# Performance work log

Measured on AMD Instinct MI355X. Metric: run time of the kernel, lower is better.

The kernel has to match this reference:

```python
import jax, jax.numpy as jnp
import numpy as np

B, C_IN, C_OUT, H, W = 4, 256, 256, 64, 64
KH = KW = 3
STRIDE = 1
PAD = 1
DIL = 1


def setup_inputs() -> dict:
    key = jax.random.key(0)
    k1, k2, k3, k4 = jax.random.split(key, 4)
    x = jax.random.normal(k1, (B, C_IN, H, W), dtype=jnp.float32)
    # torchvision layout: 2*dg*KH*KW channels, (y, x) pair per kernel tap
    offset = jax.random.normal(k2, (B, 2 * KH * KW, H, W), dtype=jnp.float32)
    fan_in = C_IN * KH * KW
    weight = jax.random.normal(k3, (C_OUT, C_IN, KH, KW), dtype=jnp.float32) / np.sqrt(fan_in)
    bias = jax.random.normal(k4, (C_OUT,), dtype=jnp.float32) * 0.01
    return {"x": x, "offset": offset, "weight": weight, "bias": bias}


def _gather_bilinear_corner(x_flat, yi, xi, h, w):
    # x_flat: [B, C, H*W]; yi/xi: [B, KK, Ho, Wo] int32
    valid = ((yi >= 0) & (yi < h) & (xi >= 0) & (xi < w)).astype(x_flat.dtype)
    idx = jnp.clip(yi, 0, h - 1) * w + jnp.clip(xi, 0, w - 1)
    b = idx.shape[0]
    g = jnp.take_along_axis(x_flat, idx.reshape(b, 1, -1), axis=2)
    return g.reshape(b, x_flat.shape[1], *yi.shape[1:]), valid


def deform_conv2d(x, offset, weight, bias):
    b, c, h, w = x.shape
    o = weight.shape[0]
    kk = KH * KW
    ho = (h + 2 * PAD - DIL * (KH - 1) - 1) // STRIDE + 1
    wo = (w + 2 * PAD - DIL * (KW - 1) - 1) // STRIDE + 1

    ky = (jnp.arange(kk, dtype=jnp.float32) // KW) * DIL  # [KK]
    kx = (jnp.arange(kk, dtype=jnp.float32) % KW) * DIL
    hs = jnp.arange(ho, dtype=jnp.float32) * STRIDE - PAD   # [Ho]
    ws = jnp.arange(wo, dtype=jnp.float32) * STRIDE - PAD   # [Wo]

    off = offset.reshape(b, kk, 2, ho, wo)
    py = hs[None, None, :, None] + ky[None, :, None, None] + off[:, :, 0]  # [B,KK,Ho,Wo]
    px = ws[None, None, None, :] + kx[None, :, None, None] + off[:, :, 1]

    y0 = jnp.floor(py)
    x0 = jnp.floor(px)
    wy1 = py - y0  # fractional parts, differentiable w.r.t. offsets
    wx1 = px - x0
    wy0 = 1.0 - wy1
    wx0 = 1.0 - wx1
    y0i = y0.astype(jnp.int32)
    x0i = x0.astype(jnp.int32)

    x_flat = x.reshape(b, c, h * w)
    corners = [
        (y0i,     x0i,     wy0 * wx0),
        (y0i,     x0i + 1, wy0 * wx1),
        (y0i + 1, x0i,     wy1 * wx0),
        (y0i + 1, x0i + 1, wy1 * wx1),
    ]
    sampled = jnp.zeros((b, c, kk, ho, wo), dtype=x.dtype)
    for yi, xi, wgt in corners:
        g, valid = _gather_bilinear_corner(x_flat, yi, xi, h, w)
        sampled = sampled + g * (wgt * valid)[:, None]

    out = jnp.einsum('bckhw,ock->bohw', sampled, weight.reshape(o, c, kk))
    return out + bias[None, :, None, None]


def reference(x, offset, weight, bias):
    return deform_conv2d(x, offset, weight, bias)
```

## Files before the change

kernel.cpp:

```cpp
#include <hip/hip_runtime.h>

typedef __bf16 bf16;
typedef __bf16 bf16x4 __attribute__((ext_vector_type(4)));
typedef __bf16 bf16x8 __attribute__((ext_vector_type(8)));
typedef float  f32x4  __attribute__((ext_vector_type(4)));

#define CIN   256
#define KK    9
#define KDIM  2304
#define KITERS 72
#define PXW   32
#define SROW  264

__device__ __forceinline__ float sread(float f) {
    return __builtin_bit_cast(float,
        __builtin_amdgcn_readfirstlane(__builtin_bit_cast(int, f)));
}

__global__ __launch_bounds__(256) void prep_k(const float* __restrict__ x,
                                              const float* __restrict__ w,
                                              bf16* __restrict__ xt,
                                              bf16* __restrict__ wq) {
    int bid = blockIdx.x;
    int tid = threadIdx.x;
    if (bid < 1024) {
        __shared__ bf16 tile[64][72];
        int pt = bid & 63, ct = (bid >> 6) & 3, b = bid >> 8;
        int lane = tid & 63, row = tid >> 6;
        const float* src = x + ((size_t)(b * 256 + ct * 64)) * 4096 + pt * 64;
        #pragma unroll
        for (int cc = row; cc < 64; cc += 4)
            tile[lane][cc] = (bf16)src[(size_t)cc * 4096 + lane];
        __syncthreads();
        bf16* dst = xt + ((size_t)(b * 4096 + pt * 64)) * 256 + ct * 64;
        int p = tid >> 3, j = tid & 7;
        #pragma unroll
        for (int pp = p; pp < 64; pp += 32)
            *reinterpret_cast<bf16x8*>(dst + (size_t)pp * 256 + j * 8) =
                *reinterpret_cast<const bf16x8*>(&tile[pp][j * 8]);
    } else {
        int idx  = (bid - 1024) * 256 + tid;
        int j    = idx & 7;
        int lane = (idx >> 3) & 63;
        int rest = idx >> 9;
        int kt   = rest % KITERS;
        int m    = rest / KITERS;
        int l16  = lane & 15;
        int quad = lane >> 4;
        int o    = m * 16 + l16;
        int k    = kt * 32 + quad * 8 + j;
        int tap  = k >> 8;
        int cc   = k & 255;
        wq[idx] = (bf16)w[(size_t)o * KDIM + cc * KK + tap];
    }
}

__global__ __launch_bounds__(512, 4) void deform_gemm_k(
    const bf16*  __restrict__ xt,
    const float* __restrict__ off,
    const bf16*  __restrict__ wq,
    const float* __restrict__ bias,
    float*       __restrict__ out) {

    __shared__ bf16 S[2][PXW][SROW];

    int tid  = threadIdx.x;
    int wave = tid >> 6;
    int lane = tid & 63;
    int quad = lane >> 4;
    int l16  = lane & 15;
    int pix0 = blockIdx.x * PXW;
    int c    = lane * 4;

    int ybase[4], xbase[4];
    unsigned base[4], ooff[4];
    #pragma unroll
    for (int i = 0; i < 4; ++i) {
        int n    = wave * 4 + i;
        int pg   = pix0 + n;
        int b    = pg >> 12;
        int pimg = pg & 4095;
        ybase[i] = pimg >> 6;
        xbase[i] = pimg & 63;
        ooff[i]  = (unsigned)b * 73728u + (unsigned)pimg;
        base[i]  = (unsigned)b * 1048576u + (unsigned)c;
    }

    f32x4 acc[2][2];
    #pragma unroll
    for (int mt = 0; mt < 2; ++mt)
        #pragma unroll
        for (int nt = 0; nt < 2; ++nt)
            acc[mt][nt] = (f32x4){0.f, 0.f, 0.f, 0.f};

    bf16x4 v[4][4];
    float  w4[4][4];

    auto gather = [&](int tap) {
        int ty = tap / 3 - 1;
        int tx = tap % 3 - 1;
        #pragma unroll
        for (int i = 0; i < 4; ++i) {
            float oy = off[(size_t)ooff[i] + (size_t)(2 * tap) * 4096];
            float ox = off[(size_t)ooff[i] + (size_t)(2 * tap + 1) * 4096];
            float py = (float)(ybase[i] + ty) + oy;
            float px = (float)(xbase[i] + tx) + ox;
            float fy = floorf(py), fx = floorf(px);
            int   y0 = (int)fy,    x0 = (int)fx;
            float wy1 = py - fy, wx1 = px - fx;
            float wy0 = 1.f - wy1, wx0 = 1.f - wx1;
            wy0 = ((unsigned)y0       < 64u) ? wy0 : 0.f;
            wy1 = ((unsigned)(y0 + 1) < 64u) ? wy1 : 0.f;
            wx0 = ((unsigned)x0       < 64u) ? wx0 : 0.f;
            wx1 = ((unsigned)(x0 + 1) < 64u) ? wx1 : 0.f;
            int yc0 = min(max(y0, 0), 63),     yc1 = min(max(y0 + 1, 0), 63);
            int xc0 = min(max(x0, 0), 63),     xc1 = min(max(x0 + 1, 0), 63);
            unsigned u0 = (unsigned)((yc0 * 64 + xc0) * 256);
            unsigned u1 = (unsigned)((yc0 * 64 + xc1) * 256);
            unsigned u2 = (unsigned)((yc1 * 64 + xc0) * 256);
            unsigned u3 = (unsigned)((yc1 * 64 + xc1) * 256);
            w4[i][0] = sread(wy0 * wx0); w4[i][1] = sread(wy0 * wx1);
            w4[i][2] = sread(wy1 * wx0); w4[i][3] = sread(wy1 * wx1);
            v[i][0] = *reinterpret_cast<const bf16x4*>(xt + base[i] + u0);
            v[i][1] = *reinterpret_cast<const bf16x4*>(xt + base[i] + u1);
            v[i][2] = *reinterpret_cast<const bf16x4*>(xt + base[i] + u2);
            v[i][3] = *reinterpret_cast<const bf16x4*>(xt + base[i] + u3);
        }
    };

    auto blend = [&](int buf) {
        #pragma unroll
        for (int i = 0; i < 4; ++i) {
            float a0 = 0.f, a1 = 0.f, a2 = 0.f, a3 = 0.f;
            #pragma unroll
            for (int j = 0; j < 4; ++j) {
                float wt = w4[i][j];
                a0 += wt * (float)v[i][j][0];
                a1 += wt * (float)v[i][j][1];
                a2 += wt * (float)v[i][j][2];
                a3 += wt * (float)v[i][j][3];
            }
            bf16x4 sv;
            sv[0] = (bf16)a0; sv[1] = (bf16)a1;
            sv[2] = (bf16)a2; sv[3] = (bf16)a3;
            *reinterpret_cast<bf16x4*>(&S[buf][wave * 4 + i][c]) = sv;
        }
    };

    auto gemm = [&](int buf, int tap) {
        const bf16* sp0 = &S[buf][l16][quad * 8];
        const bf16* sp1 = &S[buf][16 + l16][quad * 8];
        const bf16* ap0 = wq + ((size_t)((2 * wave) * KITERS + tap * 8) * 64 + lane) * 8;
        const bf16* ap1 = ap0 + (size_t)KITERS * 64 * 8;
        #pragma unroll
        for (int kki = 0; kki < 8; ++kki) {
            bf16x8 b0 = *reinterpret_cast<const bf16x8*>(sp0 + kki * 32);
            bf16x8 b1 = *reinterpret_cast<const bf16x8*>(sp1 + kki * 32);
            bf16x8 a0 = *reinterpret_cast<const bf16x8*>(ap0 + (size_t)kki * 512);
            bf16x8 a1 = *reinterpret_cast<const bf16x8*>(ap1 + (size_t)kki * 512);
            acc[0][0] = __builtin_amdgcn_mfma_f32_16x16x32_bf16(a0, b0, acc[0][0], 0, 0, 0);
            acc[0][1] = __builtin_amdgcn_mfma_f32_16x16x32_bf16(a0, b1, acc[0][1], 0, 0, 0);
            acc[1][0] = __builtin_amdgcn_mfma_f32_16x16x32_bf16(a1, b0, acc[1][0], 0, 0, 0);
            acc[1][1] = __builtin_amdgcn_mfma_f32_16x16x32_bf16(a1, b1, acc[1][1], 0, 0, 0);
        }
    };

    gather(0);
    blend(0);
    __syncthreads();

    for (int tap = 0; tap < KK; ++tap) {
        int cur = tap & 1;
        if (tap + 1 < KK) gather(tap + 1);
        gemm(cur, tap);
        if (tap + 1 < KK) blend(cur ^ 1);
        __syncthreads();
    }

    #pragma unroll
    for (int nt = 0; nt < 2; ++nt) {
        int pg   = pix0 + nt * 16 + l16;
        int b    = pg >> 12;
        int pimg = pg & 4095;
        #pragma unroll
        for (int mt = 0; mt < 2; ++mt) {
            int m = (2 * wave + mt) * 16 + quad * 4;
            float* op = out + ((size_t)(b * 256 + m)) * 4096 + pimg;
            #pragma unroll
            for (int r = 0; r < 4; ++r)
                op[(size_t)r * 4096] = acc[mt][nt][r] + bias[m + r];
        }
    }
}

extern "C" void kernel_launch(void* const* d_in, const int* in_sizes, int n_in,
                              void* d_out, int out_size, void* d_ws, size_t ws_size,
                              hipStream_t stream) {
    const float* x    = (const float*)d_in[0];
    const float* off  = (const float*)d_in[1];
    const float* w    = (const float*)d_in[2];
    const float* bias = (const float*)d_in[3];
    float* out = (float*)d_out;

    bf16* wq = (bf16*)d_ws;
    bf16* xt = (bf16*)((char*)d_ws + (size_t)589824 * 2);

    prep_k<<<3328, 256, 0, stream>>>(x, w, xt, wq);
    deform_gemm_k<<<512, 512, 0, stream>>>(xt, off, wq, bias, out);
}
```

Before: 123.6 us.

## Restructure deform GEMM to 4-wave blocks with single LDS buffer and scalarized gather

Halves the block to 256 threads, so each wave now handles 8 pixels and 4 M-tiles instead of 4 pixels and 2 M-tiles. It drops LDS double buffering in favour of a gather-then-GEMM loop with two barriers per tap, and raises the occupancy hint. Gather offsets are made wave-uniform via readfirstlane, and the block index is swizzled across batches. The aim is more blocks per CU and cheaper address math, at the cost of losing the gather/MFMA overlap within a block and adding an extra barrier per tap.

New measurement: 146.3 us. +18.4%, slower.

```diff
diff --git a/kernel.cpp b/kernel.cpp
--- a/kernel.cpp
+++ b/kernel.cpp
@@ -15,6 +15,9 @@
 __device__ __forceinline__ float sread(float f) {
     return __builtin_bit_cast(float,
         __builtin_amdgcn_readfirstlane(__builtin_bit_cast(int, f)));
+}
+__device__ __forceinline__ int sreadi(int v) {
+    return __builtin_amdgcn_readfirstlane(v);
 }
 
 __global__ __launch_bounds__(256) void prep_k(const float* __restrict__ x,
@@ -55,137 +58,121 @@
     }
 }
 
-__global__ __launch_bounds__(512, 4) void deform_gemm_k(
+__global__ __launch_bounds__(256, 6) void deform_gemm_k(
     const bf16*  __restrict__ xt,
     const float* __restrict__ off,
     const bf16*  __restrict__ wq,
     const float* __restrict__ bias,
     float*       __restrict__ out) {
 
-    __shared__ bf16 S[2][PXW][SROW];
+    __shared__ bf16 S[PXW][SROW];
 
-    int tid  = threadIdx.x;
-    int wave = tid >> 6;
-    int lane = tid & 63;
-    int quad = lane >> 4;
-    int l16  = lane & 15;
-    int pix0 = blockIdx.x * PXW;
-    int c    = lane * 4;
+    int tid   = threadIdx.x;
+    int wavei = sreadi(tid >> 6);
+    int lane  = tid & 63;
+    int quad  = lane >> 4;
+    int l16   = lane & 15;
 
-    int ybase[4], xbase[4];
-    unsigned base[4], ooff[4];
+    int bid   = blockIdx.x;
+    int pb    = ((bid & 7) << 6) | (bid >> 3);
+    int pix0  = pb * PXW;
+    int b     = pix0 >> 12;
+    int pimgb = pix0 & 4095;
+    int obase = b * 73728;
+    unsigned base = (unsigned)b * 1048576u + (unsigned)(lane * 4);
+
+    f32x4 acc[4][2];
     #pragma unroll
-    for (int i = 0; i < 4; ++i) {
-        int n    = wave * 4 + i;
-        int pg   = pix0 + n;
-        int b    = pg >> 12;
-        int pimg = pg & 4095;
-        ybase[i] = pimg >> 6;
-        xbase[i] = pimg & 63;
-        ooff[i]  = (unsigned)b * 73728u + (unsigned)pimg;
-        base[i]  = (unsigned)b * 1048576u + (unsigned)c;
-    }
-
-    f32x4 acc[2][2];
-    #pragma unroll
-    for (int mt = 0; mt < 2; ++mt)
+    for (int mt = 0; mt < 4; ++mt)
         #pragma unroll
         for (int nt = 0; nt < 2; ++nt)
             acc[mt][nt] = (f32x4){0.f, 0.f, 0.f, 0.f};
 
-    bf16x4 v[4][4];
-    float  w4[4][4];
-
-    auto gather = [&](int tap) {
+    for (int tap = 0; tap < KK; ++tap) {
         int ty = tap / 3 - 1;
         int tx = tap % 3 - 1;
+
         #pragma unroll
-        for (int i = 0; i < 4; ++i) {
-            float oy = off[(size_t)ooff[i] + (size_t)(2 * tap) * 4096];
-            float ox = off[(size_t)ooff[i] + (size_t)(2 * tap + 1) * 4096];
-            float py = (float)(ybase[i] + ty) + oy;
-            float px = (float)(xbase[i] + tx) + ox;
-            float fy = floorf(py), fx = floorf(px);
-            int   y0 = (int)fy,    x0 = (int)fx;
-            float wy1 = py - fy, wx1 = px - fx;
-            float wy0 = 1.f - wy1, wx0 = 1.f - wx1;
-            wy0 = ((unsigned)y0       < 64u) ? wy0 : 0.f;
-            wy1 = ((unsigned)(y0 + 1) < 64u) ? wy1 : 0.f;
-            wx0 = ((unsigned)x0       < 64u) ? wx0 : 0.f;
-            wx1 = ((unsigned)(x0 + 1) < 64u) ? wx1 : 0.f;
-            int yc0 = min(max(y0, 0), 63),     yc1 = min(max(y0 + 1, 0), 63);
-            int xc0 = min(max(x0, 0), 63),     xc1 = min(max(x0 + 1, 0), 63);
-            unsigned u0 = (unsigned)((yc0 * 64 + xc0) * 256);
-            unsigned u1 = (unsigned)((yc0 * 64 + xc1) * 256);
-            unsigned u2 = (unsigned)((yc1 * 64 + xc0) * 256);
-            unsigned u3 = (unsigned)((yc1 * 64 + xc1) * 256);
-            w4[i][0] = sread(wy0 * wx0); w4[i][1] = sread(wy0 * wx1);
-            w4[i][2] = sread(wy1 * wx0); w4[i][3] = sread(wy1 * wx1);
-            v[i][0] = *reinterpret_cast<const bf16x4*>(xt + base[i] + u0);
-            v[i][1] = *reinterpret_cast<const bf16x4*>(xt + base[i] + u1);
-            v[i][2] = *reinterpret_cast<const bf16x4*>(xt + base[i] + u2);
-            v[i][3] = *reinterpret_cast<const bf16x4*>(xt + base[i] + u3);
+        for (int g = 0; g < 2; ++g) {
+            int u[4][4];
+            float wt[4][4];
+            #pragma unroll
+            for (int i = 0; i < 4; ++i) {
+                int n    = wavei * 8 + g * 4 + i;
+                int pimg = pimgb + n;
+                float oy = off[obase + pimg + (2 * tap) * 4096];
+                float ox = off[obase + pimg + (2 * tap + 1) * 4096];
+                float py = (float)((pimg >> 6) + ty) + oy;
+                float px = (float)((pimg & 63) + tx) + ox;
+                float fy = floorf(py), fx = floorf(px);
+                int   y0 = (int)fy,    x0 = (int)fx;
+                float wy1 = py - fy, wx1 = px - fx;
+                float wy0 = 1.f - wy1, wx0 = 1.f - wx1;
+                wy0 = ((unsigned)y0       < 64u) ? wy0 : 0.f;
+                wy1 = ((unsigned)(y0 + 1) < 64u) ? wy1 : 0.f;
+                wx0 = ((unsigned)x0       < 64u) ? wx0 : 0.f;
+                wx1 = ((unsigned)(x0 + 1) < 64u) ? wx1 : 0.f;
+                int yc0 = min(max(y0, 0), 63),     yc1 = min(max(y0 + 1, 0), 63);
+                int xc0 = min(max(x0, 0), 63),     xc1 = min(max(x0 + 1, 0), 63);
+                u[i][0] = sreadi((yc0 * 64 + xc0) * 256);
+                u[i][1] = sreadi((yc0 * 64 + xc1) * 256);
+                u[i][2] = sreadi((yc1 * 64 + xc0) * 256);
+                u[i][3] = sreadi((yc1 * 64 + xc1) * 256);
+                wt[i][0] = sread(wy0 * wx0); wt[i][1] = sread(wy0 * wx1);
+                wt[i][2] = sread(wy1 * wx0); wt[i][3] = sread(wy1 * wx1);
+            }
+            bf16x4 v[4][4];
+            #pragma unroll
+            for (int i = 0; i < 4; ++i)
+                #pragma unroll
+                for (int j = 0; j < 4; ++j)
+                    v[i][j] = *reinterpret_cast<const bf16x4*>(xt + base + (unsigned)u[i][j]);
+            #pragma unroll
+            for (int i = 0; i < 4; ++i) {
+                float a0 = 0.f, a1 = 0.f, a2 = 0.f, a3 = 0.f;
+                #pragma unroll
+                for (int j = 0; j < 4; ++j) {
+                    float wgt = wt[i][j];
+                    a0 += wgt * (float)v[i][j][0];
+                    a1 += wgt * (float)v[i][j][1];
+                    a2 += wgt * (float)v[i][j][2];
+                    a3 += wgt * (float)v[i][j][3];
+                }
+                bf16x4 sv;
+                sv[0] = (bf16)a0; sv[1] = (bf16)a1;
+                sv[2] = (bf16)a2; sv[3] = (bf16)a3;
+                *reinterpret_cast<bf16x4*>(&S[wavei * 8 + g * 4 + i][lane * 4]) = sv;
+            }
         }
-    };
+        __syncthreads();
 
-    auto blend = [&](int buf) {
-        #pragma unroll
-        for (int i = 0; i < 4; ++i) {
-            float a0 = 0.f, a1 = 0.f, a2 = 0.f, a3 = 0.f;
-            #pragma unroll
-            for (int j = 0; j < 4; ++j) {
-                float wt = w4[i][j];
-                a0 += wt * (float)v[i][j][0];
-                a1 += wt * (float)v[i][j][1];
-                a2 += wt * (float)v[i][j][2];
-                a3 += wt * (float)v[i][j][3];
-            }
-            bf16x4 sv;
-            sv[0] = (bf16)a0; sv[1] = (bf16)a1;
-            sv[2] = (bf16)a2; sv[3] = (bf16)a3;
-            *reinterpret_cast<bf16x4*>(&S[buf][wave * 4 + i][c]) = sv;
-        }
-    };
-
-    auto gemm = [&](int buf, int tap) {
-        const bf16* sp0 = &S[buf][l16][quad * 8];
-        const bf16* sp1 = &S[buf][16 + l16][quad * 8];
-        const bf16* ap0 = wq + ((size_t)((2 * wave) * KITERS + tap * 8) * 64 + lane) * 8;
-        const bf16* ap1 = ap0 + (size_t)KITERS * 64 * 8;
+        const bf16* sp0 = &S[l16][quad * 8];
+        const bf16* sp1 = &S[16 + l16][quad * 8];
         #pragma unroll
         for (int kki = 0; kki < 8; ++kki) {
             bf16x8 b0 = *reinterpret_cast<const bf16x8*>(sp0 + kki * 32);
             bf16x8 b1 = *reinterpret_cast<const bf16x8*>(sp1 + kki * 32);
-            bf16x8 a0 = *reinterpret_cast<const bf16x8*>(ap0 + (size_t)kki * 512);
-            bf16x8 a1 = *reinterpret_cast<const bf16x8*>(ap1 + (size_t)kki * 512);
-            acc[0][0] = __builtin_amdgcn_mfma_f32_16x16x32_bf16(a0, b0, acc[0][0], 0, 0, 0);
-            acc[0][1] = __builtin_amdgcn_mfma_f32_16x16x32_bf16(a0, b1, acc[0][1], 0, 0, 0);
-            acc[1][0] = __builtin_amdgcn_mfma_f32_16x16x32_bf16(a1, b0, acc[1][0], 0, 0, 0);
-            acc[1][1] = __builtin_amdgcn_mfma_f32_16x16x32_bf16(a1, b1, acc[1][1], 0, 0, 0);
+            #pragma unroll
+            for (int mt = 0; mt < 4; ++mt) {
+                const bf16* ap = wq +
+                    ((size_t)(((wavei * 4 + mt) * KITERS + tap * 8 + kki) * 64 + lane)) * 8;
+                bf16x8 a = *reinterpret_cast<const bf16x8*>(ap);
+                acc[mt][0] = __builtin_amdgcn_mfma_f32_16x16x32_bf16(a, b0, acc[mt][0], 0, 0, 0);
+                acc[mt][1] = __builtin_amdgcn_mfma_f32_16x16x32_bf16(a, b1, acc[mt][1], 0, 0, 0);
+            }
         }
-    };
-
-    gather(0);
-    blend(0);
-    __syncthreads();
-
-    for (int tap = 0; tap < KK; ++tap) {
-        int cur = tap & 1;
-        if (tap + 1 < KK) gather(tap + 1);
-        gemm(cur, tap);
-        if (tap + 1 < KK) blend(cur ^ 1);
         __syncthreads();
     }
 
     #pragma unroll
     for (int nt = 0; nt < 2; ++nt) {
         int pg   = pix0 + nt * 16 + l16;
-        int b    = pg >> 12;
+        int bb   = pg >> 12;
         int pimg = pg & 4095;
         #pragma unroll
-        for (int mt = 0; mt < 2; ++mt) {
-            int m = (2 * wave + mt) * 16 + quad * 4;
-            float* op = out + ((size_t)(b * 256 + m)) * 4096 + pimg;
+        for (int mt = 0; mt < 4; ++mt) {
+            int m = (wavei * 4 + mt) * 16 + quad * 4;
+            float* op = out + ((size_t)(bb * 256 + m)) * 4096 + pimg;
             #pragma unroll
             for (int r = 0; r < 4; ++r)
                 op[(size_t)r * 4096] = acc[mt][nt][r] + bias[m + r];
@@ -206,5 +193,5 @@
     bf16* xt = (bf16*)((char*)d_ws + (size_t)589824 * 2);
 
     prep_k<<<3328, 256, 0, stream>>>(x, w, xt, wq);
-    deform_gemm_k<<<512, 512, 0, stream>>>(xt, off, wq, bias, out);
+    deform_gemm_k<<<512, 256, 0, stream>>>(xt, off, wq, bias, out);
 }
```
